# Optimization experiments

Hardware: AMD Instinct MI355X
Metric: run time of the kernel (lower is better)

Reference implementation:

```python
import jax, jax.numpy as jnp
import numpy as np

B, T, H = 2, 4096, 2048
NH, HD, INTER, K = 16, 128, 8192, 3
BASE = 10000.0
EPS = 1e-6


def setup_inputs() -> dict:
    key = jax.random.key(0)
    ks = jax.random.split(key, 10)
    s = 0.02
    return {
        "hidden_states": jax.random.normal(ks[0], (B, T, H), jnp.float32),
        "position_ids": jnp.tile(jnp.arange(T, dtype=jnp.int32)[None, :], (B, 1)),
        "conv_w": jax.random.normal(ks[1], (H, H, K), jnp.float32) * s,  # OIH
        "conv_b": jnp.zeros((H,), jnp.float32),
        "wq": jax.random.normal(ks[2], (H, NH * HD), jnp.float32) * s,
        "wv": jax.random.normal(ks[3], (H, NH * HD), jnp.float32) * s,
        "w_dt": jax.random.normal(ks[4], (H, NH), jnp.float32) * s,
        "b_dt": jnp.zeros((NH,), jnp.float32),
        "A_log": jnp.full((NH,), -4.0, jnp.float32),
        "dt_bias": jnp.full((NH,), -2.0, jnp.float32),
        "wo": jax.random.normal(ks[5], (NH * HD, H), jnp.float32) * s,
        "w1": jax.random.normal(ks[6], (H, INTER), jnp.float32) * s,
        "w2": jax.random.normal(ks[7], (INTER, H), jnp.float32) * s,
        "norm1_w": jnp.ones((H,), jnp.float32),
        "norm2_w": jnp.ones((H,), jnp.float32),
    }


def _rmsnorm(x, w):
    return x * jax.lax.rsqrt(jnp.mean(x * x, axis=-1, keepdims=True) + EPS) * w


def _causal_conv(x, conv_w, conv_b):
    # x: [B,T,H] -> NCH conv with left pad (causal)
    xc = jnp.transpose(x, (0, 2, 1))  # [B,H,T]
    y = jax.lax.conv_general_dilated(
        xc, conv_w, window_strides=(1,), padding=[(K - 1, 0)],
        dimension_numbers=("NCH", "OIH", "NCH"))
    y = y + conv_b[None, :, None]
    return jnp.transpose(y, (0, 2, 1))  # [B,T,H]


def _rope(q, position_ids):
    # q: [B,NH,T,HD]; matches the torch interleaved-rotate + concatenated cos/sin
    inv_freq = 1.0 / (BASE ** (jnp.arange(0, HD, 2, dtype=jnp.float32) / HD))
    freqs = position_ids.astype(jnp.float32)[..., None] * inv_freq  # [B,T,HD/2]
    emb = jnp.concatenate([freqs, freqs], axis=-1)                   # [B,T,HD]
    cos = jnp.cos(emb)[:, None]  # [B,1,T,HD]
    sin = jnp.sin(emb)[:, None]
    x1, x2 = q[..., ::2], q[..., 1::2]
    x_rot = jnp.stack([-x2, x1], axis=-1).reshape(q.shape)
    return q * cos + x_rot * sin


def _gated_deltanet(h, position_ids, conv_w, conv_b, wq, wv, w_dt, b_dt, A_log, dt_bias, wo):
    x = _causal_conv(h, conv_w, conv_b)  # [B,T,H]
    q = (x @ wq).reshape(B, T, NH, HD).transpose(0, 2, 1, 3)  # [B,NH,T,HD]
    v = (x @ wv).reshape(B, T, NH, HD).transpose(0, 2, 1, 3)
    q = _rope(q, position_ids)
    dt_raw = (h @ w_dt + b_dt).transpose(0, 2, 1)  # [B,NH,T]
    dt = jax.nn.softplus(dt_raw + dt_bias[None, :, None])
    A = -jnp.exp(A_log)[None, :, None]
    alpha = jnp.exp(A * dt)
    beta = dt
    p = jnp.cumprod(alpha, axis=2)                 # [B,NH,T]
    u = beta[..., None] * v / (p[..., None] + EPS)  # [B,NH,T,HD]
    s = jnp.cumsum(u, axis=2)
    state = p[..., None] * s
    out = (q * state).transpose(0, 2, 1, 3).reshape(B, T, NH * HD)
    return out @ wo


def reference(hidden_states, position_ids, conv_w, conv_b, wq, wv, w_dt, b_dt,
              A_log, dt_bias, wo, w1, w2, norm1_w, norm2_w):
    # pre-norm residual decoder layer: attn block then MLP block
    attn_in = _rmsnorm(hidden_states, norm1_w)
    h = hidden_states + _gated_deltanet(attn_in, position_ids, conv_w, conv_b,
                                        wq, wv, w_dt, b_dt, A_log, dt_bias, wo)
    mlp_in = _rmsnorm(h, norm2_w)
    out = h + (jax.nn.silu(mlp_in @ w1) @ w2)
    return out
```

## Files before the change

### kernel.cpp

```cpp
#include <hip/hip_runtime.h>
#include <stdint.h>

#define T_DIM 4096
#define H_DIM 2048
#define NHEADS 16
#define HD_DIM 128
#define INTER_DIM 8192
#define B_DIM 2
#define MROWS (B_DIM * T_DIM)
#define NCHUNK 32
#define CHUNK (T_DIM / NCHUNK)

typedef unsigned short ushort_t;
typedef _Float16 f16x8 __attribute__((ext_vector_type(8)));
typedef __attribute__((ext_vector_type(4))) float f32x4;

__device__ __forceinline__ ushort_t f2h(float f) {
    union { _Float16 h; ushort_t u; } x;
    x.h = (_Float16)f;
    return x.u;
}
__device__ __forceinline__ float h2f(ushort_t u) {
    union { ushort_t u; _Float16 h; } x;
    x.u = u;
    return (float)x.h;
}

__device__ __forceinline__ void stage16(const ushort_t* g, ushort_t* lbase) {
#if __has_builtin(__builtin_amdgcn_global_load_lds)
    __builtin_amdgcn_global_load_lds(
        (__attribute__((address_space(1))) unsigned int*)g,
        (__attribute__((address_space(3))) unsigned int*)lbase,
        16, 0, 0);
#else
    ((f16x8*)lbase)[threadIdx.x & 63] = *(const f16x8*)g;
#endif
}

__device__ __forceinline__ void vm4_barrier() {
    asm volatile("s_waitcnt vmcnt(4)\n\ts_barrier" ::: "memory");
}
__device__ __forceinline__ void vm2_barrier() {
    asm volatile("s_waitcnt vmcnt(2)\n\ts_barrier" ::: "memory");
}
__device__ __forceinline__ void vm0_barrier() {
    asm volatile("s_waitcnt vmcnt(0)\n\ts_barrier" ::: "memory");
}


#define PH_STAGE_A0(W)                                                        \
    if (STG) {                                                                \
        stage16(gAs,          &Asm[(W) * 16384 + wave * 1024]);               \
        stage16(gAs + lda8,   &Asm[(W) * 16384 + wave * 1024 + 512]);         \
    }
#define PH_STAGE_B0(W)                                                        \
    if (STG) {                                                                \
        stage16(gBs,          &Bsm[(W) * 16384 + wave * 1024]);               \
        stage16(gBs + ldb8,   &Bsm[(W) * 16384 + wave * 1024 + 512]);         \
    }
#define PH_STAGE_B1(W)                                                        \
    if (STG) {                                                                \
        stage16(gBs + ldb128, &Bsm[(W) * 16384 + 8192 + wave * 1024]);        \
        stage16(gBs + ldb136, &Bsm[(W) * 16384 + 8192 + wave * 1024 + 512]);  \
    }
#define PH_STAGE_A1(W)                                                        \
    if (STG) {                                                                \
        stage16(gAs + lda128, &Asm[(W) * 16384 + 8192 + wave * 1024]);        \
        stage16(gAs + lda136, &Asm[(W) * 16384 + 8192 + wave * 1024 + 512]);  \
    }

#define LDS_A(R, HA)                                                          \
    _Pragma("unroll")                                                         \
    for (int mi = 0; mi < 4; ++mi) {                                          \
        af[mi * 2 + 0] = *(const f16x8*)&Asm[(R) * 16384 + (HA) * 8192 +      \
                                             mi * 1024 + rdA0];               \
        af[mi * 2 + 1] = *(const f16x8*)&Asm[(R) * 16384 + (HA) * 8192 +      \
                                             mi * 1024 + rdA1];               \
    }
#define LDS_B(R, HB)                                                          \
    _Pragma("unroll")                                                         \
    for (int ni = 0; ni < 2; ++ni) {                                          \
        bf[(HB) * 4 + ni * 2 + 0] =                                           \
            *(const f16x8*)&Bsm[(R) * 16384 + (HB) * 8192 + ni * 1024 + rdB0];\
        bf[(HB) * 4 + ni * 2 + 1] =                                           \
            *(const f16x8*)&Bsm[(R) * 16384 + (HB) * 8192 + ni * 1024 + rdB1];\
    }
#define MF(HA, HB)                                                            \
    __builtin_amdgcn_s_setprio(1);                                            \
    _Pragma("unroll")                                                         \
    for (int mi = 0; mi < 4; ++mi)                                            \
    _Pragma("unroll")                                                         \
    for (int ni = 0; ni < 2; ++ni)                                            \
    _Pragma("unroll")                                                         \
    for (int kk = 0; kk < 2; ++kk)                                            \
        acc[(HA) * 4 + mi][(HB) * 2 + ni] =                                   \
            __builtin_amdgcn_mfma_f32_16x16x32_f16(                           \
                af[mi * 2 + kk], bf[(HB) * 4 + ni * 2 + kk],                  \
                acc[(HA) * 4 + mi][(HB) * 2 + ni], 0, 0, 0);                  \
    __builtin_amdgcn_s_setprio(0);

#define ADVANCE()                                                             \
    {                                                                         \
        gAs += 64;                                                            \
        ++ts;                                                                 \
        if (SHIFTS == 3 && (ts & (KT - 1)) == 0 && ts < NT) {                 \
            gBs = (ts == KT) ? gBp1 : gBp2;                                   \
        } else {                                                              \
            gBs += 64;                                                        \
        }                                                                     \
    }

#define TILE(R, STG)                                                          \
    {                                                                         \
        PH_STAGE_A0(1 - (R))                                                  \
        PH_STAGE_B0(1 - (R))                                                  \
        LDS_A(R, 0)                                                           \
        LDS_B(R, 0)                                                           \
        LDS_B(R, 1)                                                           \
        MF(0, 0)                                                              \
        MF(0, 1)                                                              \
        if (STG) vm4_barrier(); else vm0_barrier();                           \
        PH_STAGE_B1(1 - (R))                                                  \
        PH_STAGE_A1(1 - (R))                                                  \
        LDS_A(R, 1)                                                           \
        MF(1, 0)                                                              \
        MF(1, 1)                                                              \
        if (STG) {                                                            \
            vm2_barrier();                                                    \
            ADVANCE()                                                         \
        }                                                                     \
    }

template <int EPI, int SHIFTS>
__global__ __launch_bounds__(512, 2) void gemm256(
    const ushort_t* __restrict__ A,
    const ushort_t* __restrict__ B0,
    const ushort_t* __restrict__ B1,
    const ushort_t* __restrict__ B2,
    const float* __restrict__ bias,
    const float* addsrc,
    float* outf,
    ushort_t* outb,
    int M, int N, int K, int lda, int ldb)
{
    __shared__ __align__(16) ushort_t Asm[2 * 16384];
    __shared__ __align__(16) ushort_t Bsm[2 * 16384];

    const int tid  = threadIdx.x;
    const int lane = tid & 63;
    const int wave = tid >> 6;

    const int nwg = gridDim.x * gridDim.y;
    const int bid = blockIdx.y * gridDim.x + blockIdx.x;
    const int swz = (bid & 7) * (nwg >> 3) + (bid >> 3);
    const int gxl = 31 - __clz((int)gridDim.x);
    const int bx  = swz & ((int)gridDim.x - 1);
    const int by  = swz >> gxl;

    const int m0 = by * 256;
    const int n0 = bx * 256;
    const int wm2 = (wave >> 2) * 64;
    const int wn2 = (wave & 3) * 32;
    const int m16 = lane & 15;
    const int q4  = lane >> 4;
    const int l7  = lane & 7;
    const int srow = lane >> 3;
    const int soct = (lane & 7) ^ srow;

    const int KT = K >> 6;
    const int NT = SHIFTS * KT;

    const int rdA0 = (wm2 + m16) * 64 + (q4 ^ l7) * 8;
    const int rdA1 = rdA0 ^ 32;
    const int rdB0 = (wn2 + m16) * 64 + (q4 ^ l7) * 8;
    const int rdB1 = rdB0 ^ 32;

    const size_t lda8 = (size_t)lda * 8,  lda128 = (size_t)lda * 128, lda136 = (size_t)lda * 136;
    const size_t ldb8 = (size_t)ldb * 8,  ldb128 = (size_t)ldb * 128, ldb136 = (size_t)ldb * 136;
    const size_t athr = (size_t)(wave * 16 + srow) * lda + soct * 8;
    const size_t bthr = (size_t)(wave * 16 + srow) * ldb + soct * 8;
    const ushort_t* gAs;
    if (SHIFTS == 3) {
        int b = m0 >> 12;
        gAs = A + (size_t)(m0 + 2 * b) * lda + athr;
    } else {
        gAs = A + (size_t)m0 * lda + athr;
    }
    const ushort_t* gBs  = B0 + (size_t)n0 * ldb + bthr;
    const ushort_t* gBp1 = (SHIFTS == 3) ? (B1 + (size_t)n0 * ldb + bthr) : nullptr;
    const ushort_t* gBp2 = (SHIFTS == 3) ? (B2 + (size_t)n0 * ldb + bthr) : nullptr;
    int ts = 0;

    f32x4 acc[8][4];
#pragma unroll
    for (int i = 0; i < 8; i++)
#pragma unroll
        for (int j = 0; j < 4; j++)
#pragma unroll
            for (int r = 0; r < 4; r++) acc[i][j][r] = 0.f;

    f16x8 af[8];
    f16x8 bf[8];

    {
        const bool STG = true;
        PH_STAGE_A0(0)
        PH_STAGE_B0(0)
        PH_STAGE_B1(0)
        PH_STAGE_A1(0)
        ADVANCE()
    }
    vm2_barrier();

    for (int t = 0; t < NT - 2; t += 2) {
        { const bool STG = true; TILE(0, STG) }
        { const bool STG = true; TILE(1, STG) }
    }
    { const bool STG = true;  TILE(0, STG) }
    { const bool STG = false; TILE(1, STG) }

#pragma unroll
    for (int a = 0; a < 8; ++a) {
        const int ha = a >> 2, mi = a & 3;
#pragma unroll
        for (int b = 0; b < 4; ++b) {
            const int hb = b >> 1, ni = b & 1;
            const int col = n0 + hb * 128 + wn2 + ni * 16 + m16;
#pragma unroll
            for (int r = 0; r < 4; ++r) {
                const int row = m0 + ha * 128 + wm2 + mi * 16 + q4 * 4 + r;
                const size_t idx = (size_t)row * N + col;
                float v = acc[a][b][r];
                if (EPI == 1) {
                    outf[idx] = v;
                } else if (EPI == 2) {
                    outb[idx] = f2h(v + bias[col]);
                } else if (EPI == 3) {
                    outf[idx] = addsrc[idx] + v;
                } else if (EPI == 4) {
                    outb[idx] = f2h(v / (1.f + expf(-v)));
                } else if (EPI == 5) {
                    outb[idx] = f2h(v);
                }
            }
        }
    }
}

#undef PH_STAGE_A0
#undef PH_STAGE_B0
#undef PH_STAGE_B1
#undef PH_STAGE_A1
#undef LDS_A
#undef LDS_B
#undef MF
#undef ADVANCE
#undef TILE

__global__ void transpose_to_f16(const float* __restrict__ in, ushort_t* __restrict__ out,
                                 int R, int C) {
    __shared__ float tile[32][33];
    int c0 = blockIdx.x * 32, r0 = blockIdx.y * 32;
    int tx = threadIdx.x, ty = threadIdx.y;
#pragma unroll
    for (int j = 0; j < 32; j += 8)
        tile[ty + j][tx] = in[(size_t)(r0 + ty + j) * C + c0 + tx];
    __syncthreads();
#pragma unroll
    for (int j = 0; j < 32; j += 8)
        out[(size_t)(c0 + ty + j) * R + r0 + tx] = f2h(tile[tx][ty + j]);
}

__global__ void conv_w_convert(const float* __restrict__ cw, ushort_t* __restrict__ w0,
                               ushort_t* __restrict__ w1, ushort_t* __restrict__ w2) {
    int gid = blockIdx.x * 256 + threadIdx.x;
    const float* p = cw + (size_t)gid * 3;
    w0[gid] = f2h(p[0]);
    w1[gid] = f2h(p[1]);
    w2[gid] = f2h(p[2]);
}

__global__ __launch_bounds__(256) void rmsnorm_kernel(const float* __restrict__ x,
                                                      const float* __restrict__ w,
                                                      ushort_t* __restrict__ out, int pad) {
    int r = blockIdx.x;
    int tid = threadIdx.x;
    const float* row = x + (size_t)r * H_DIM;
    float xs[8];
    *(float4*)&xs[0] = *(const float4*)&row[tid * 8];
    *(float4*)&xs[4] = *(const float4*)&row[tid * 8 + 4];
    float ss = 0.f;
#pragma unroll
    for (int e = 0; e < 8; e++) ss += xs[e] * xs[e];
#pragma unroll
    for (int o = 32; o >= 1; o >>= 1) ss += __shfl_down(ss, o, 64);
    __shared__ float red[4];
    if ((tid & 63) == 0) red[tid >> 6] = ss;
    __syncthreads();
    float rs = rsqrtf((red[0] + red[1] + red[2] + red[3]) * (1.f / 2048.f) + 1e-6f);
    float ws[8];
    *(float4*)&ws[0] = *(const float4*)&w[tid * 8];
    *(float4*)&ws[4] = *(const float4*)&w[tid * 8 + 4];
    ushort_t* orow;
    if (pad) {
        int b = r >> 12, t = r & 4095;
        orow = out + ((size_t)b * (T_DIM + 2) + 2 + t) * H_DIM;
        if (t == 0) {
            ushort_t* pz = out + (size_t)b * (T_DIM + 2) * H_DIM;
            for (int e = tid; e < 2 * H_DIM; e += 256) pz[e] = 0;
        }
    } else {
        orow = out + (size_t)r * H_DIM;
    }
#pragma unroll
    for (int e = 0; e < 8; e++) orow[tid * 8 + e] = f2h(xs[e] * rs * ws[e]);
}

__global__ __launch_bounds__(256) void dt_kernel(const ushort_t* __restrict__ apad,
                                                 const float* __restrict__ wdt,
                                                 const float* __restrict__ bdt,
                                                 const float* __restrict__ dtb,
                                                 float* __restrict__ beta_arr) {
    int r = blockIdx.x;
    int b = r >> 12, t = r & 4095;
    int tid = threadIdx.x, lane = tid & 63, wv = tid >> 6;
    const ushort_t* row = apad + ((size_t)b * (T_DIM + 2) + 2 + t) * H_DIM;
    float acc[16];
#pragma unroll
    for (int nh = 0; nh < 16; nh++) acc[nh] = 0.f;
    f16x8 xv = *(const f16x8*)&row[tid * 8];
#pragma unroll
    for (int e = 0; e < 8; e++) {
        float x = (float)xv[e];
        const float* wrow = wdt + (size_t)(tid * 8 + e) * 16;
#pragma unroll
        for (int nh = 0; nh < 16; nh++) acc[nh] += x * wrow[nh];
    }
    __shared__ float part[4][16];
#pragma unroll
    for (int nh = 0; nh < 16; nh++) {
        float v = acc[nh];
#pragma unroll
        for (int o = 32; o >= 1; o >>= 1) v += __shfl_down(v, o, 64);
        if (lane == 0) part[wv][nh] = v;
    }
    __syncthreads();
    if (tid < 16) {
        float v = part[0][tid] + part[1][tid] + part[2][tid] + part[3][tid];
        float x = v + bdt[tid] + dtb[tid];
        float dt = (x > 20.f) ? x : log1pf(expf(x));
        beta_arr[(size_t)(b * 16 + tid) * T_DIM + t] = dt;
    }
}

__global__ __launch_bounds__(256) void scan_prep(const float* __restrict__ beta_arr,
                                                 const float* __restrict__ A_log,
                                                 float* __restrict__ p_arr,
                                                 float* __restrict__ c_arr) {
    int bh = blockIdx.x;
    int nh = bh & 15;
    int tid = threadIdx.x;
    float Ac = -expf(A_log[nh]);
    size_t base = (size_t)bh * T_DIM;
    float bet[16], pref[16];
    float run = 0.f;
#pragma unroll
    for (int j = 0; j < 16; j++) {
        bet[j] = beta_arr[base + tid * 16 + j];
        run += Ac * bet[j];
        pref[j] = run;
    }
    __shared__ float red[256];
    red[tid] = run;
    __syncthreads();
    if (tid == 0) {
        float a = 0.f;
        for (int i = 0; i < 256; i++) { float x = red[i]; red[i] = a; a += x; }
    }
    __syncthreads();
    float off = red[tid];
#pragma unroll
    for (int j = 0; j < 16; j++) {
        float p = expf(off + pref[j]);
        p_arr[base + tid * 16 + j] = p;
        c_arr[base + tid * 16 + j] = bet[j] / (p + 1e-6f);
    }
}

__global__ __launch_bounds__(128) void scan_partial(const float* __restrict__ c_arr,
                                                    const ushort_t* __restrict__ v_buf,
                                                    float* __restrict__ csum) {
    int blk = blockIdx.x;
    int ch = blk & (NCHUNK - 1), bh = blk >> 5;
    int b = bh >> 4, nh = bh & 15;
    int tid = threadIdx.x;
    int t0 = ch * CHUNK;
    __shared__ float cs[CHUNK];
    cs[tid] = c_arr[(size_t)bh * T_DIM + t0 + tid];
    __syncthreads();
    float s = 0.f;
    const ushort_t* vbase = v_buf + ((size_t)(b * T_DIM + t0) * 16 + nh) * 128 + tid;
    for (int tt = 0; tt < CHUNK; tt++) s += cs[tt] * h2f(vbase[(size_t)tt * 2048]);
    csum[(size_t)blk * 128 + tid] = s;
}

__global__ __launch_bounds__(128) void scan_combine(const float* __restrict__ csum,
                                                    float* __restrict__ cpref) {
    int bh = blockIdx.x;
    int tid = threadIdx.x;
    float run = 0.f;
    for (int ch = 0; ch < NCHUNK; ch++) {
        size_t i = ((size_t)bh * NCHUNK + ch) * 128 + tid;
        cpref[i] = run;
        run += csum[i];
    }
}

__global__ __launch_bounds__(128) void scan_final(const float* __restrict__ c_arr,
                                                  const float* __restrict__ p_arr,
                                                  const ushort_t* __restrict__ v_buf,
                                                  const ushort_t* __restrict__ q_buf,
                                                  const float* __restrict__ cpref,
                                                  ushort_t* __restrict__ y_head) {
    int blk = blockIdx.x;
    int ch = blk & (NCHUNK - 1), bh = blk >> 5;
    int b = bh >> 4, nh = bh & 15;
    int tid = threadIdx.x;
    int t0 = ch * CHUNK;
    __shared__ float cs[CHUNK], ps[CHUNK];
    cs[tid] = c_arr[(size_t)bh * T_DIM + t0 + tid];
    ps[tid] = p_arr[(size_t)bh * T_DIM + t0 + tid];
    __syncthreads();
    float s = cpref[(size_t)blk * 128 + tid];
    size_t vb = ((size_t)(b * T_DIM + t0) * 16 + nh) * 128 + tid;
    for (int tt = 0; tt < CHUNK; tt++) {
        size_t vi = vb + (size_t)tt * 2048;
        s += cs[tt] * h2f(v_buf[vi]);
        float y = h2f(q_buf[vi]) * (ps[tt] * s);
        y_head[vi] = f2h(y);
    }
}

__global__ __launch_bounds__(256) void rope_f16(ushort_t* __restrict__ q,
                                                const int* __restrict__ pos_ids) {
    int gid = blockIdx.x * 256 + threadIdx.x;
    int j = gid & 63;
    int rest = gid >> 6;
    int bt = rest >> 4;
    size_t idx = (size_t)bt * 2048 + (size_t)(rest & 15) * 128 + 2 * j;
    float pos = (float)pos_ids[bt];
    const float LN = 0.14391157f;
    int d0 = 2 * j, d1 = 2 * j + 1;
    float a0 = pos * expf(-(float)(d0 & 63) * LN);
    float a1 = pos * expf(-(float)(d1 & 63) * LN);
    float q0 = h2f(q[idx]), q1 = h2f(q[idx + 1]);
    q[idx]     = f2h(q0 * cosf(a0) - q1 * sinf(a0));
    q[idx + 1] = f2h(q1 * cosf(a1) + q0 * sinf(a1));
}

extern "C" void kernel_launch(void* const* d_in, const int* in_sizes, int n_in,
                              void* d_out, int out_size, void* d_ws, size_t ws_size,
                              hipStream_t stream) {
    (void)in_sizes; (void)n_in; (void)out_size;
    const float* hidden  = (const float*)d_in[0];
    const int*   pos_ids = (const int*)d_in[1];
    const float* conv_w  = (const float*)d_in[2];
    const float* conv_b  = (const float*)d_in[3];
    const float* wq      = (const float*)d_in[4];
    const float* wv      = (const float*)d_in[5];
    const float* w_dt    = (const float*)d_in[6];
    const float* b_dt    = (const float*)d_in[7];
    const float* A_log   = (const float*)d_in[8];
    const float* dt_bias = (const float*)d_in[9];
    const float* wo      = (const float*)d_in[10];
    const float* w1      = (const float*)d_in[11];
    const float* w2      = (const float*)d_in[12];
    const float* n1w     = (const float*)d_in[13];
    const float* n2w     = (const float*)d_in[14];
    float* out = (float*)d_out;

    constexpr size_t MB8 = 8ull * 1024 * 1024;
    constexpr size_t SCAN_SM = 524288;
    constexpr size_t R0   = 0;
    constexpr size_t R0sz = 10 * MB8;
    constexpr size_t R1   = R0 + R0sz;
    constexpr size_t R1sz = 8 * MB8;
    constexpr size_t R2   = R1 + R1sz;
    constexpr size_t R2sz = (size_t)B_DIM * (T_DIM + 2) * H_DIM * 2;
    constexpr size_t R3   = R2 + R2sz;
    constexpr size_t R3sz = 4 * MB8;
    constexpr size_t R4   = R3 + R3sz;
    constexpr size_t R4sz = 4 * MB8;
    constexpr size_t R5   = R4 + R4sz;
    constexpr size_t R5sz = 5 * SCAN_SM;
    constexpr size_t NEED = R5 + R5sz;
    if (ws_size < NEED) return;

    char* w = (char*)d_ws;
    ushort_t* wc0    = (ushort_t*)(w + R0 + 0 * MB8);
    ushort_t* wc1    = (ushort_t*)(w + R0 + 1 * MB8);
    ushort_t* wc2    = (ushort_t*)(w + R0 + 2 * MB8);
    ushort_t* wq_t   = (ushort_t*)(w + R0 + 3 * MB8);
    ushort_t* wv_t   = (ushort_t*)(w + R0 + 4 * MB8);
    ushort_t* wo_t   = (ushort_t*)(w + R0 + 5 * MB8);
    ushort_t* xb     = (ushort_t*)(w + R0 + 6 * MB8);
    ushort_t* a_half = (ushort_t*)(w + R0);
    ushort_t* qb     = (ushort_t*)(w + R1);
    ushort_t* vb     = (ushort_t*)(w + R1 + 4 * MB8);
    float*    h_buf  = (float*)(w + R1);
    ushort_t* apad   = (ushort_t*)(w + R2);
    ushort_t* w1_t   = (ushort_t*)(w + R3);
    ushort_t* w2_t   = (ushort_t*)(w + R4);
    float*    beta   = (float*)(w + R5 + 0 * SCAN_SM);
    float*    parr   = (float*)(w + R5 + 1 * SCAN_SM);
    float*    carr   = (float*)(w + R5 + 2 * SCAN_SM);
    float*    csum   = (float*)(w + R5 + 3 * SCAN_SM);
    float*    cprf   = (float*)(w + R5 + 4 * SCAN_SM);
    ushort_t* mlp_in = apad;
    ushort_t* y_head = xb;

    conv_w_convert<<<(2048 * 2048) / 256, 256, 0, stream>>>(conv_w, wc0, wc1, wc2);
    transpose_to_f16<<<dim3(64, 64), dim3(32, 8), 0, stream>>>(wq, wq_t, 2048, 2048);
    transpose_to_f16<<<dim3(64, 64), dim3(32, 8), 0, stream>>>(wv, wv_t, 2048, 2048);
    transpose_to_f16<<<dim3(64, 64), dim3(32, 8), 0, stream>>>(wo, wo_t, 2048, 2048);
    transpose_to_f16<<<dim3(256, 64), dim3(32, 8), 0, stream>>>(w1, w1_t, 2048, 8192);
    transpose_to_f16<<<dim3(64, 256), dim3(32, 8), 0, stream>>>(w2, w2_t, 8192, 2048);

    rmsnorm_kernel<<<MROWS, 256, 0, stream>>>(hidden, n1w, apad, 1);
    dt_kernel<<<MROWS, 256, 0, stream>>>(apad, w_dt, b_dt, dt_bias, beta);
    scan_prep<<<B_DIM * NHEADS, 256, 0, stream>>>(beta, A_log, parr, carr);

    gemm256<2, 3><<<dim3(8, 32), 512, 0, stream>>>(
        apad, wc0, wc1, wc2, conv_b, nullptr, nullptr, xb,
        MROWS, 2048, 2048, 2048, 2048);
    gemm256<5, 1><<<dim3(8, 32), 512, 0, stream>>>(
        xb, wq_t, wq_t, wq_t, nullptr, nullptr, nullptr, qb,
        MROWS, 2048, 2048, 2048, 2048);
    gemm256<5, 1><<<dim3(8, 32), 512, 0, stream>>>(
        xb, wv_t, wv_t, wv_t, nullptr, nullptr, nullptr, vb,
        MROWS, 2048, 2048, 2048, 2048);
    rope_f16<<<(MROWS * NHEADS * 64) / 256, 256, 0, stream>>>(qb, pos_ids);

    scan_partial<<<B_DIM * NHEADS * NCHUNK, 128, 0, stream>>>(carr, vb, csum);
    scan_combine<<<B_DIM * NHEADS, 128, 0, stream>>>(csum, cprf);
    scan_final<<<B_DIM * NHEADS * NCHUNK, 128, 0, stream>>>(carr, parr, vb, qb, cprf, y_head);

    gemm256<3, 1><<<dim3(8, 32), 512, 0, stream>>>(
        y_head, wo_t, wo_t, wo_t, nullptr, hidden, h_buf, nullptr,
        MROWS, 2048, 2048, 2048, 2048);
    rmsnorm_kernel<<<MROWS, 256, 0, stream>>>(h_buf, n2w, mlp_in, 0);

    for (int ha = 0; ha < 2; ha++) {
        gemm256<4, 1><<<dim3(16, 32), 512, 0, stream>>>(
            mlp_in, w1_t + (size_t)ha * 4096 * 2048, nullptr, nullptr,
            nullptr, nullptr, nullptr, a_half,
            MROWS, 4096, 2048, 2048, 2048);
        gemm256<3, 1><<<dim3(8, 32), 512, 0, stream>>>(
            a_half, w2_t + (size_t)ha * 4096, nullptr, nullptr,
            nullptr, (ha == 0) ? h_buf : out, out, nullptr,
            MROWS, 2048, 4096, 4096, 8192);
    }
}
```

Before: 1.650 ms.

## Load B operand fragments directly from global into registers, bypassing LDS

The GEMM no longer stages the B tile through shared memory. Each wave loads its own B fragments straight from global memory into registers, one tile ahead, and only A is double-buffered in LDS. The goal is to halve LDS traffic and footprint and to drop a barrier phase per tile. The cost is that B rows shared across waves with the same column slice are fetched redundantly from global/L2, and the loads are only 16-byte chunks per lane with a strided row pattern, which may give poorer coalescing. The vmcnt accounting also changes to wait for 8 outstanding loads.

```diff
diff --git a/kernel.cpp b/kernel.cpp
--- a/kernel.cpp
+++ b/kernel.cpp
@@ -37,14 +37,8 @@
 #endif
 }
 
-__device__ __forceinline__ void vm4_barrier() {
-    asm volatile("s_waitcnt vmcnt(4)\n\ts_barrier" ::: "memory");
-}
-__device__ __forceinline__ void vm2_barrier() {
-    asm volatile("s_waitcnt vmcnt(2)\n\ts_barrier" ::: "memory");
-}
-__device__ __forceinline__ void vm0_barrier() {
-    asm volatile("s_waitcnt vmcnt(0)\n\ts_barrier" ::: "memory");
+__device__ __forceinline__ void vm8_barrier() {
+    asm volatile("s_waitcnt vmcnt(8)\n\ts_barrier" ::: "memory");
 }
 
 
@@ -52,16 +46,6 @@
     if (STG) {                                                                \
         stage16(gAs,          &Asm[(W) * 16384 + wave * 1024]);               \
         stage16(gAs + lda8,   &Asm[(W) * 16384 + wave * 1024 + 512]);         \
-    }
-#define PH_STAGE_B0(W)                                                        \
-    if (STG) {                                                                \
-        stage16(gBs,          &Bsm[(W) * 16384 + wave * 1024]);               \
-        stage16(gBs + ldb8,   &Bsm[(W) * 16384 + wave * 1024 + 512]);         \
-    }
-#define PH_STAGE_B1(W)                                                        \
-    if (STG) {                                                                \
-        stage16(gBs + ldb128, &Bsm[(W) * 16384 + 8192 + wave * 1024]);        \
-        stage16(gBs + ldb136, &Bsm[(W) * 16384 + 8192 + wave * 1024 + 512]);  \
     }
 #define PH_STAGE_A1(W)                                                        \
     if (STG) {                                                                \
@@ -77,14 +61,22 @@
         af[mi * 2 + 1] = *(const f16x8*)&Asm[(R) * 16384 + (HA) * 8192 +      \
                                              mi * 1024 + rdA1];               \
     }
-#define LDS_B(R, HB)                                                          \
-    _Pragma("unroll")                                                         \
-    for (int ni = 0; ni < 2; ++ni) {                                          \
-        bf[(HB) * 4 + ni * 2 + 0] =                                           \
-            *(const f16x8*)&Bsm[(R) * 16384 + (HB) * 8192 + ni * 1024 + rdB0];\
-        bf[(HB) * 4 + ni * 2 + 1] =                                           \
-            *(const f16x8*)&Bsm[(R) * 16384 + (HB) * 8192 + ni * 1024 + rdB1];\
-    }
+
+#define BF1_LOAD()                                                            \
+    if (STG) {                                                                \
+        bf[4] = *(const f16x8*)gB2;                                           \
+        bf[5] = *(const f16x8*)(gB2 + 32);                                    \
+        bf[6] = *(const f16x8*)gB3;                                           \
+        bf[7] = *(const f16x8*)(gB3 + 32);                                    \
+    }
+#define BF0_LOAD()                                                            \
+    if (STG) {                                                                \
+        bf[0] = *(const f16x8*)gB0;                                           \
+        bf[1] = *(const f16x8*)(gB0 + 32);                                    \
+        bf[2] = *(const f16x8*)gB1;                                           \
+        bf[3] = *(const f16x8*)(gB1 + 32);                                    \
+    }
+
 #define MF(HA, HB)                                                            \
     __builtin_amdgcn_s_setprio(1);                                            \
     _Pragma("unroll")                                                         \
@@ -103,30 +95,32 @@
     {                                                                         \
         gAs += 64;                                                            \
         ++ts;                                                                 \
-        if (SHIFTS == 3 && (ts & (KT - 1)) == 0 && ts < NT) {                 \
-            gBs = (ts == KT) ? gBp1 : gBp2;                                   \
+        if (SHIFTS == 3 && ts < NT && (ts & (KT - 1)) == 0) {                 \
+            const ptrdiff_t hop =                                             \
+                ((ts == KT) ? (B1 - B0) : (B2 - B1)) -                        \
+                (ptrdiff_t)(KT - 1) * 64;                                     \
+            gB0 += hop; gB1 += hop; gB2 += hop; gB3 += hop;                   \
         } else {                                                              \
-            gBs += 64;                                                        \
+            gB0 += 64; gB1 += 64; gB2 += 64; gB3 += 64;                       \
         }                                                                     \
     }
 
-#define TILE(R, STG)                                                          \
+#define TILE(R, STG_)                                                         \
     {                                                                         \
+        const bool STG = STG_;                                                \
         PH_STAGE_A0(1 - (R))                                                  \
-        PH_STAGE_B0(1 - (R))                                                  \
+        PH_STAGE_A1(1 - (R))                                                  \
+        if (STG) __builtin_amdgcn_sched_barrier(0);                           \
         LDS_A(R, 0)                                                           \
-        LDS_B(R, 0)                                                           \
-        LDS_B(R, 1)                                                           \
+        MF(0, 1)                                                              \
         MF(0, 0)                                                              \
-        MF(0, 1)                                                              \
-        if (STG) vm4_barrier(); else vm0_barrier();                           \
-        PH_STAGE_B1(1 - (R))                                                  \
-        PH_STAGE_A1(1 - (R))                                                  \
         LDS_A(R, 1)                                                           \
+        MF(1, 1)                                                              \
+        BF1_LOAD()                                                            \
         MF(1, 0)                                                              \
-        MF(1, 1)                                                              \
+        BF0_LOAD()                                                            \
         if (STG) {                                                            \
-            vm2_barrier();                                                    \
+            vm8_barrier();                                                    \
             ADVANCE()                                                         \
         }                                                                     \
     }
@@ -144,7 +138,6 @@
     int M, int N, int K, int lda, int ldb)
 {
     __shared__ __align__(16) ushort_t Asm[2 * 16384];
-    __shared__ __align__(16) ushort_t Bsm[2 * 16384];
 
     const int tid  = threadIdx.x;
     const int lane = tid & 63;
@@ -172,13 +165,9 @@
 
     const int rdA0 = (wm2 + m16) * 64 + (q4 ^ l7) * 8;
     const int rdA1 = rdA0 ^ 32;
-    const int rdB0 = (wn2 + m16) * 64 + (q4 ^ l7) * 8;
-    const int rdB1 = rdB0 ^ 32;
-
-    const size_t lda8 = (size_t)lda * 8,  lda128 = (size_t)lda * 128, lda136 = (size_t)lda * 136;
-    const size_t ldb8 = (size_t)ldb * 8,  ldb128 = (size_t)ldb * 128, ldb136 = (size_t)ldb * 136;
+
+    const size_t lda8 = (size_t)lda * 8, lda128 = (size_t)lda * 128, lda136 = (size_t)lda * 136;
     const size_t athr = (size_t)(wave * 16 + srow) * lda + soct * 8;
-    const size_t bthr = (size_t)(wave * 16 + srow) * ldb + soct * 8;
     const ushort_t* gAs;
     if (SHIFTS == 3) {
         int b = m0 >> 12;
@@ -186,9 +175,11 @@
     } else {
         gAs = A + (size_t)m0 * lda + athr;
     }
-    const ushort_t* gBs  = B0 + (size_t)n0 * ldb + bthr;
-    const ushort_t* gBp1 = (SHIFTS == 3) ? (B1 + (size_t)n0 * ldb + bthr) : nullptr;
-    const ushort_t* gBp2 = (SHIFTS == 3) ? (B2 + (size_t)n0 * ldb + bthr) : nullptr;
+
+    const ushort_t* gB0 = B0 + (size_t)(n0 + wn2 + m16) * ldb + q4 * 8;
+    const ushort_t* gB1 = gB0 + (size_t)16 * ldb;
+    const ushort_t* gB2 = gB0 + (size_t)128 * ldb;
+    const ushort_t* gB3 = gB0 + (size_t)144 * ldb;
     int ts = 0;
 
     f32x4 acc[8][4];
@@ -205,19 +196,20 @@
     {
         const bool STG = true;
         PH_STAGE_A0(0)
-        PH_STAGE_B0(0)
-        PH_STAGE_B1(0)
         PH_STAGE_A1(0)
+        __builtin_amdgcn_sched_barrier(0);
+        BF1_LOAD()
+        BF0_LOAD()
         ADVANCE()
     }
-    vm2_barrier();
+    vm8_barrier();
 
     for (int t = 0; t < NT - 2; t += 2) {
-        { const bool STG = true; TILE(0, STG) }
-        { const bool STG = true; TILE(1, STG) }
-    }
-    { const bool STG = true;  TILE(0, STG) }
-    { const bool STG = false; TILE(1, STG) }
+        TILE(0, true)
+        TILE(1, true)
+    }
+    TILE(0, true)
+    TILE(1, false)
 
 #pragma unroll
     for (int a = 0; a < 8; ++a) {
@@ -248,11 +240,10 @@
 }
 
 #undef PH_STAGE_A0
-#undef PH_STAGE_B0
-#undef PH_STAGE_B1
 #undef PH_STAGE_A1
 #undef LDS_A
-#undef LDS_B
+#undef BF1_LOAD
+#undef BF0_LOAD
 #undef MF
 #undef ADVANCE
 #undef TILE
```

Result: slower. 1.939 ms (+17.5%).

## Restructure GEMM main loop into fine-grained 8-phase LDS/global prefetch schedule

Applied to the files above, without the earlier changes.

Rewrites the 256x256 GEMM inner loop as a two-tile iteration split into eight phases. Each phase issues one quarter of the next tile's global-to-LDS staging, does its LDS fragment reads, waits on lgkmcnt, then runs an MFMA block, with s_barrier separating the phases. The aim is to interleave memory traffic with MFMA work more evenly and keep more loads in flight (vmcnt 6 instead of 2/4), hiding global latency. In exchange it adds many more workgroup barriers per tile and more complex pointer advancement across the shifted B operands, which risks stalls and correctness errors in the staging order.

```diff
diff --git a/kernel.cpp b/kernel.cpp
--- a/kernel.cpp
+++ b/kernel.cpp
@@ -37,36 +37,38 @@
 #endif
 }
 
-__device__ __forceinline__ void vm4_barrier() {
-    asm volatile("s_waitcnt vmcnt(4)\n\ts_barrier" ::: "memory");
-}
-__device__ __forceinline__ void vm2_barrier() {
-    asm volatile("s_waitcnt vmcnt(2)\n\ts_barrier" ::: "memory");
-}
-__device__ __forceinline__ void vm0_barrier() {
+__device__ __forceinline__ void barx() { asm volatile("s_barrier" ::: "memory"); }
+__device__ __forceinline__ void vm6_bar() {
+    asm volatile("s_waitcnt vmcnt(6)\n\ts_barrier" ::: "memory");
+}
+__device__ __forceinline__ void vm0_bar() {
     asm volatile("s_waitcnt vmcnt(0)\n\ts_barrier" ::: "memory");
 }
-
-
-#define PH_STAGE_A0(W)                                                        \
-    if (STG) {                                                                \
-        stage16(gAs,          &Asm[(W) * 16384 + wave * 1024]);               \
-        stage16(gAs + lda8,   &Asm[(W) * 16384 + wave * 1024 + 512]);         \
-    }
-#define PH_STAGE_B0(W)                                                        \
-    if (STG) {                                                                \
-        stage16(gBs,          &Bsm[(W) * 16384 + wave * 1024]);               \
-        stage16(gBs + ldb8,   &Bsm[(W) * 16384 + wave * 1024 + 512]);         \
-    }
-#define PH_STAGE_B1(W)                                                        \
-    if (STG) {                                                                \
-        stage16(gBs + ldb128, &Bsm[(W) * 16384 + 8192 + wave * 1024]);        \
-        stage16(gBs + ldb136, &Bsm[(W) * 16384 + 8192 + wave * 1024 + 512]);  \
-    }
-#define PH_STAGE_A1(W)                                                        \
-    if (STG) {                                                                \
-        stage16(gAs + lda128, &Asm[(W) * 16384 + 8192 + wave * 1024]);        \
-        stage16(gAs + lda136, &Asm[(W) * 16384 + 8192 + wave * 1024 + 512]);  \
+__device__ __forceinline__ void lgkm0() {
+    asm volatile("s_waitcnt lgkmcnt(0)" ::: "memory");
+    __builtin_amdgcn_sched_barrier(0);
+}
+
+
+#define ST_ALO(W, GA)                                                         \
+    {                                                                         \
+        stage16((GA),        &Asm[(W) * 16384 + wave * 1024]);                \
+        stage16((GA) + lda8, &Asm[(W) * 16384 + wave * 1024 + 512]);          \
+    }
+#define ST_AHI(W, GA)                                                         \
+    {                                                                         \
+        stage16((GA) + lda128, &Asm[(W) * 16384 + 8192 + wave * 1024]);       \
+        stage16((GA) + lda136, &Asm[(W) * 16384 + 8192 + wave * 1024 + 512]); \
+    }
+#define ST_BLO(W, GB)                                                         \
+    {                                                                         \
+        stage16((GB),        &Bsm[(W) * 16384 + wave * 1024]);                \
+        stage16((GB) + ldb8, &Bsm[(W) * 16384 + wave * 1024 + 512]);          \
+    }
+#define ST_BHI(W, GB)                                                         \
+    {                                                                         \
+        stage16((GB) + ldb128, &Bsm[(W) * 16384 + 8192 + wave * 1024]);       \
+        stage16((GB) + ldb136, &Bsm[(W) * 16384 + 8192 + wave * 1024 + 512]); \
     }
 
 #define LDS_A(R, HA)                                                          \
@@ -99,36 +101,69 @@
                 acc[(HA) * 4 + mi][(HB) * 2 + ni], 0, 0, 0);                  \
     __builtin_amdgcn_s_setprio(0);
 
-#define ADVANCE()                                                             \
+#define ADV_B()                                                               \
     {                                                                         \
-        gAs += 64;                                                            \
         ++ts;                                                                 \
-        if (SHIFTS == 3 && (ts & (KT - 1)) == 0 && ts < NT) {                 \
-            gBs = (ts == KT) ? gBp1 : gBp2;                                   \
+        if (SHIFTS == 3 && ts < NT && (ts & (KT - 1)) == 0) {                 \
+            gB = ((ts == KT) ? gBp1 : gBp2) + (size_t)(ts & (KT - 1)) * 64;   \
+            gB += (size_t)(ts - ((ts >= 2 * KT) ? 2 * KT : KT)) * 64;         \
         } else {                                                              \
-            gBs += 64;                                                        \
+            gB += 64;                                                         \
         }                                                                     \
     }
 
-#define TILE(R, STG)                                                          \
+#define ITER(STG)                                                             \
     {                                                                         \
-        PH_STAGE_A0(1 - (R))                                                  \
-        PH_STAGE_B0(1 - (R))                                                  \
-        LDS_A(R, 0)                                                           \
-        LDS_B(R, 0)                                                           \
-        LDS_B(R, 1)                                                           \
+                                         \
+        LDS_A(0, 0)                                                           \
+        LDS_B(0, 0)                                                           \
+        ST_AHI(1, gA)                            \
+        barx(); lgkm0();                                                      \
         MF(0, 0)                                                              \
+        barx();                                                               \
+                                                       \
+        LDS_B(0, 1)                                                           \
+        if (STG) ST_ALO(0, gA + 64)                             \
+        barx(); lgkm0();                                                      \
         MF(0, 1)                                                              \
-        if (STG) vm4_barrier(); else vm0_barrier();                           \
-        PH_STAGE_B1(1 - (R))                                                  \
-        PH_STAGE_A1(1 - (R))                                                  \
-        LDS_A(R, 1)                                                           \
+        barx();                                                               \
+                                                       \
+        LDS_A(0, 1)                                                           \
+        if (STG) ST_BLO(0, gB)                                  \
+        barx(); lgkm0();                                                      \
         MF(1, 0)                                                              \
+        barx();                                                               \
+                                          \
+        if (STG) { ST_BHI(0, gB) vm6_bar(); } else { vm0_bar(); }             \
+        lgkm0();                                                              \
         MF(1, 1)                                                              \
-        if (STG) {                                                            \
-            vm2_barrier();                                                    \
-            ADVANCE()                                                         \
-        }                                                                     \
+        barx();                                                               \
+        if (STG) ADV_B()                                       \
+                                       \
+        LDS_A(1, 0)                                                           \
+        LDS_B(1, 0)                                                           \
+        if (STG) ST_AHI(0, gA + 64)                             \
+        barx(); lgkm0();                                                      \
+        MF(0, 0)                                                              \
+        barx();                                                               \
+                                                                     \
+        LDS_B(1, 1)                                                           \
+        if (STG) ST_ALO(1, gA + 128)                            \
+        barx(); lgkm0();                                                      \
+        MF(0, 1)                                                              \
+        barx();                                                               \
+                                                                     \
+        LDS_A(1, 1)                                                           \
+        if (STG) ST_BLO(1, gB)                                  \
+        barx(); lgkm0();                                                      \
+        MF(1, 0)                                                              \
+        barx();                                                               \
+                                                        \
+        if (STG) { ST_BHI(1, gB) vm6_bar(); } else { barx(); }                \
+        lgkm0();                                                              \
+        MF(1, 1)                                                              \
+        barx();                                                               \
+        if (STG) { ADV_B() gA += 128; }                                       \
     }
 
 template <int EPI, int SHIFTS>
@@ -169,24 +204,25 @@
 
     const int KT = K >> 6;
     const int NT = SHIFTS * KT;
+    const int NIT = NT >> 1;
 
     const int rdA0 = (wm2 + m16) * 64 + (q4 ^ l7) * 8;
     const int rdA1 = rdA0 ^ 32;
     const int rdB0 = (wn2 + m16) * 64 + (q4 ^ l7) * 8;
     const int rdB1 = rdB0 ^ 32;
 
-    const size_t lda8 = (size_t)lda * 8,  lda128 = (size_t)lda * 128, lda136 = (size_t)lda * 136;
-    const size_t ldb8 = (size_t)ldb * 8,  ldb128 = (size_t)ldb * 128, ldb136 = (size_t)ldb * 136;
+    const size_t lda8 = (size_t)lda * 8, lda128 = (size_t)lda * 128, lda136 = (size_t)lda * 136;
+    const size_t ldb8 = (size_t)ldb * 8, ldb128 = (size_t)ldb * 128, ldb136 = (size_t)ldb * 136;
     const size_t athr = (size_t)(wave * 16 + srow) * lda + soct * 8;
     const size_t bthr = (size_t)(wave * 16 + srow) * ldb + soct * 8;
-    const ushort_t* gAs;
+    const ushort_t* gA;
     if (SHIFTS == 3) {
         int b = m0 >> 12;
-        gAs = A + (size_t)(m0 + 2 * b) * lda + athr;
+        gA = A + (size_t)(m0 + 2 * b) * lda + athr;
     } else {
-        gAs = A + (size_t)m0 * lda + athr;
-    }
-    const ushort_t* gBs  = B0 + (size_t)n0 * ldb + bthr;
+        gA = A + (size_t)m0 * lda + athr;
+    }
+    const ushort_t* gB  = B0 + (size_t)n0 * ldb + bthr;
     const ushort_t* gBp1 = (SHIFTS == 3) ? (B1 + (size_t)n0 * ldb + bthr) : nullptr;
     const ushort_t* gBp2 = (SHIFTS == 3) ? (B2 + (size_t)n0 * ldb + bthr) : nullptr;
     int ts = 0;
@@ -202,22 +238,22 @@
     f16x8 af[8];
     f16x8 bf[8];
 
-    {
-        const bool STG = true;
-        PH_STAGE_A0(0)
-        PH_STAGE_B0(0)
-        PH_STAGE_B1(0)
-        PH_STAGE_A1(0)
-        ADVANCE()
-    }
-    vm2_barrier();
-
-    for (int t = 0; t < NT - 2; t += 2) {
-        { const bool STG = true; TILE(0, STG) }
-        { const bool STG = true; TILE(1, STG) }
-    }
-    { const bool STG = true;  TILE(0, STG) }
-    { const bool STG = false; TILE(1, STG) }
+    ST_ALO(0, gA)
+    ST_BLO(0, gB)
+    ST_BHI(0, gB)
+    ST_AHI(0, gA)
+    ST_ALO(1, gA + 64)
+    ADV_B()
+    ST_BLO(1, gB)
+    ST_BHI(1, gB)
+    ADV_B()
+    vm6_bar();
+    gA += 64;
+
+    for (int it = 0; it < NIT - 1; ++it) {
+        ITER(1)
+    }
+    ITER(0)
 
 #pragma unroll
     for (int a = 0; a < 8; ++a) {
@@ -247,15 +283,15 @@
     }
 }
 
-#undef PH_STAGE_A0
-#undef PH_STAGE_B0
-#undef PH_STAGE_B1
-#undef PH_STAGE_A1
+#undef ST_ALO
+#undef ST_AHI
+#undef ST_BLO
+#undef ST_BHI
 #undef LDS_A
 #undef LDS_B
 #undef MF
-#undef ADVANCE
-#undef TILE
+#undef ADV_B
+#undef ITER
 
 __global__ void transpose_to_f16(const float* __restrict__ in, ushort_t* __restrict__ out,
                                  int R, int C) {
```

After: 1.633 ms. Within noise of the previous version (-1.0%).
